# Performance work log

Measured on AMD Instinct MI355X. Metric: run time of the kernel, lower is better.

## Reference

```python
import jax, jax.numpy as jnp
import numpy as np

B, N, M, D = 1, 16384, 16384, 3
CHUNK = 2048          # x tile size for the online-min KNN pass
NN_WEIGHT = 1.0       # self.nn_weight
# both_ways=False, free_weight=0, ch_normals_K=0 -> only cham_x branch is active


def setup_inputs() -> dict:
    key = jax.random.key(0)
    k1, k2, k3 = jax.random.split(key, 3)
    # LiDAR-like point clouds, scaled to a ~20 m scene extent
    pc1 = jax.random.normal(k1, (B, N, D), dtype=jnp.float32) * 10.0
    est_flow = jax.random.normal(k2, (B, N, D), dtype=jnp.float32) * 0.1
    pc2 = jax.random.normal(k3, (B, M, D), dtype=jnp.float32) * 10.0
    return {"pc1": pc1, "est_flow": est_flow, "pc2": pc2}


def _knn1_l1_dists(x, y):
    """Per-point min L1 distance from x [N,3] to y [M,3], tiled over x.

    Equivalent to knn_points(x, y, K=1, norm=1).dists[..., 0] without
    materializing the full [N, M] distance matrix.
    """
    n = x.shape[0]
    x_tiles = x.reshape(n // CHUNK, CHUNK, D)

    def tile_min(xc):  # xc: [CHUNK, 3]
        d = jnp.sum(jnp.abs(xc[:, None, :] - y[None, :, :]), axis=-1)  # [CHUNK, M]
        return jnp.min(d, axis=-1)                                     # [CHUNK]

    return jax.lax.map(tile_min, x_tiles).reshape(n)


def reference(pc1, est_flow, pc2):
    x = pc1 + est_flow                                   # deformed cloud [B,N,3]
    cham_x = jax.vmap(_knn1_l1_dists)(x, pc2)            # [B, N]
    cham_y = jnp.float32(0.0)                            # both_ways=False
    freespace_loss = jnp.zeros_like(cham_x)              # free_weight == 0 branch
    chamf_loss = NN_WEIGHT * (cham_x.mean() + cham_y)    # free_weight * 0 omitted
    return (chamf_loss, freespace_loss)
```

## Files before the change

### kernel.cpp

```cpp
#include <hip/hip_runtime.h>


#define TPB 256
#define RB 8
#define PTS_PER_BLOCK (TPB * RB)
#define MSEG 128

__global__ __launch_bounds__(TPB) void chamfer_kernel(
    const float* __restrict__ pc1, const float* __restrict__ flow,
    const float* __restrict__ pc2, unsigned* __restrict__ minbits,
    int N, int M) {
    __shared__ float ysx[MSEG], ysy[MSEG], ysz[MSEG];

    const int t  = threadIdx.x;
    const int y0 = blockIdx.y * MSEG;
    const int len = (M - y0 < MSEG) ? (M - y0) : MSEG;

    for (int j = t; j < len; j += TPB) {
        const int g = y0 + j;
        ysx[j] = pc2[3 * g];
        ysy[j] = pc2[3 * g + 1];
        ysz[j] = pc2[3 * g + 2];
    }

    const int ibase = blockIdx.x * PTS_PER_BLOCK + t;
    float ax[RB], ay[RB], az[RB];
#pragma unroll
    for (int r = 0; r < RB; ++r) {
        const int i = ibase + r * TPB;
        const int ic = (i < N) ? i : (N - 1);
        ax[r] = pc1[3 * ic]     + flow[3 * ic];
        ay[r] = pc1[3 * ic + 1] + flow[3 * ic + 1];
        az[r] = pc1[3 * ic + 2] + flow[3 * ic + 2];
    }
    __syncthreads();

    float m[RB];
#pragma unroll
    for (int r = 0; r < RB; ++r) m[r] = 3.0e38f;

    if ((len & 3) == 0) {
        const float4* __restrict__ X4 = (const float4*)ysx;
        const float4* __restrict__ Y4 = (const float4*)ysy;
        const float4* __restrict__ Z4 = (const float4*)ysz;
#pragma unroll 2
        for (int q = 0; q < len / 4; ++q) {
            const float4 YX = X4[q];
            const float4 YY = Y4[q];
            const float4 YZ = Z4[q];
#pragma unroll
            for (int r = 0; r < RB; ++r) {
                const float d0 = fabsf(ax[r] - YX.x) + fabsf(ay[r] - YY.x) + fabsf(az[r] - YZ.x);
                const float d1 = fabsf(ax[r] - YX.y) + fabsf(ay[r] - YY.y) + fabsf(az[r] - YZ.y);
                const float d2 = fabsf(ax[r] - YX.z) + fabsf(ay[r] - YY.z) + fabsf(az[r] - YZ.z);
                const float d3 = fabsf(ax[r] - YX.w) + fabsf(ay[r] - YY.w) + fabsf(az[r] - YZ.w);
                m[r] = fminf(fminf(m[r], d0), d1);
                m[r] = fminf(fminf(m[r], d2), d3);
            }
        }
    } else {
        for (int j = 0; j < len; ++j) {
            const float yx = ysx[j], yy = ysy[j], yz = ysz[j];
#pragma unroll
            for (int r = 0; r < RB; ++r)
                m[r] = fminf(m[r], fabsf(ax[r] - yx) + fabsf(ay[r] - yy) + fabsf(az[r] - yz));
        }
    }

#pragma unroll
    for (int r = 0; r < RB; ++r) {
        const int i = ibase + r * TPB;
        if (i < N) atomicMin(&minbits[i], __float_as_uint(m[r]));
    }
}

__global__ __launch_bounds__(1024) void reduce_kernel(
    const unsigned* __restrict__ minbits, float* __restrict__ out, int N) {
    float s = 0.0f;
    const uint4* p = (const uint4*)minbits;
    for (int k = threadIdx.x; k < N / 4; k += 1024) {
        uint4 v = p[k];
        s += __uint_as_float(v.x) + __uint_as_float(v.y) +
             __uint_as_float(v.z) + __uint_as_float(v.w);
    }
    for (int k = (N / 4) * 4 + threadIdx.x; k < N; k += 1024)
        s += __uint_as_float(minbits[k]);
#pragma unroll
    for (int off = 32; off > 0; off >>= 1) s += __shfl_down(s, off, 64);
    __shared__ float ls[16];
    const int wid = threadIdx.x >> 6, lane = threadIdx.x & 63;
    if (lane == 0) ls[wid] = s;
    __syncthreads();
    if (threadIdx.x == 0) {
        float tot = 0.0f;
        for (int w = 0; w < 16; ++w) tot += ls[w];
        out[0] = tot / (float)N;
    }
}

extern "C" void kernel_launch(void* const* d_in, const int* in_sizes, int n_in,
                              void* d_out, int out_size, void* d_ws, size_t ws_size,
                              hipStream_t stream) {
    const float* pc1  = (const float*)d_in[0];
    const float* flow = (const float*)d_in[1];
    const float* pc2  = (const float*)d_in[2];
    float* out = (float*)d_out;

    const int N = in_sizes[0] / 3;
    const int M = in_sizes[2] / 3;

    unsigned* minbits = (unsigned*)d_ws;

    hipMemsetAsync(d_out, 0, (size_t)out_size * sizeof(float), stream);
    hipMemsetAsync(minbits, 0x7F, (size_t)N * sizeof(unsigned), stream);

    const int nbN    = (N + PTS_PER_BLOCK - 1) / PTS_PER_BLOCK;
    const int msplit = (M + MSEG - 1) / MSEG;

    chamfer_kernel<<<dim3(nbN, msplit), TPB, 0, stream>>>(pc1, flow, pc2, minbits, N, M);
    reduce_kernel<<<1, 1024, 0, stream>>>(minbits, out, N);
}
```

Before: 49.97 us.

## Use inline-asm abs-add/min3 distance kernel with software-pipelined LDS loads and RB=4

Replaces the compiler-generated L1 distance loop with inline GCN assembly that folds the abs into v_add operands and combines two distances per v_min3. The loop now loads the next float4 group from LDS while the current one is computed. Per-thread rows drop from 8 to 4 and launch bounds request 8 blocks per CU, trading register reuse of the y tile for higher occupancy. The shared arrays are padded so the prefetch one group past the end stays in bounds.

```diff
diff --git a/kernel.cpp b/kernel.cpp
--- a/kernel.cpp
+++ b/kernel.cpp
@@ -2,15 +2,45 @@
 
 
 #define TPB 256
-#define RB 8
+#define RB 4
 #define PTS_PER_BLOCK (TPB * RB)
 #define MSEG 128
 
-__global__ __launch_bounds__(TPB) void chamfer_kernel(
+#define DIST2(MR, AXv, AYv, AZv, Y0X, Y0Y, Y0Z, Y1X, Y1Y, Y1Z)            \
+  {                                                                        \
+    float t0, t1, t2, t3, t4;                                              \
+    asm("v_sub_f32 %1, %6, %9\n\t"                                         \
+        "v_sub_f32 %2, %7, %10\n\t"                                        \
+        "v_sub_f32 %3, %8, %11\n\t"                                        \
+        "v_sub_f32 %4, %6, %12\n\t"                                        \
+        "v_sub_f32 %5, %7, %13\n\t"                                        \
+        "v_add_f32 %1, |%1|, |%2|\n\t"                                     \
+        "v_sub_f32 %2, %8, %14\n\t"                                        \
+        "v_add_f32 %4, |%4|, |%5|\n\t"                                     \
+        "v_add_f32 %1, %1, |%3|\n\t"                                       \
+        "v_add_f32 %4, %4, |%2|\n\t"                                       \
+        "v_min3_f32 %0, %0, %1, %4"                                        \
+        : "+v"(MR), "=&v"(t0), "=&v"(t1), "=&v"(t2), "=&v"(t3), "=&v"(t4)  \
+        : "v"(AXv), "v"(AYv), "v"(AZv),                                    \
+          "v"(Y0X), "v"(Y0Y), "v"(Y0Z), "v"(Y1X), "v"(Y1Y), "v"(Y1Z));    \
+  }
+
+#define DIST8(Q4X, Q4Y, Q4Z)                                               \
+  {                                                                        \
+    _Pragma("unroll")                                                      \
+    for (int r = 0; r < RB; ++r) {                                         \
+      DIST2(m[r], ax[r], ay[r], az[r],                                     \
+            Q4X.x, Q4Y.x, Q4Z.x, Q4X.y, Q4Y.y, Q4Z.y);                     \
+      DIST2(m[r], ax[r], ay[r], az[r],                                     \
+            Q4X.z, Q4Y.z, Q4Z.z, Q4X.w, Q4Y.w, Q4Z.w);                     \
+    }                                                                      \
+  }
+
+__global__ __launch_bounds__(TPB, 8) void chamfer_kernel(
     const float* __restrict__ pc1, const float* __restrict__ flow,
     const float* __restrict__ pc2, unsigned* __restrict__ minbits,
     int N, int M) {
-    __shared__ float ysx[MSEG], ysy[MSEG], ysz[MSEG];
+    __shared__ float ysx[MSEG + 4], ysy[MSEG + 4], ysz[MSEG + 4];
 
     const int t  = threadIdx.x;
     const int y0 = blockIdx.y * MSEG;
@@ -39,24 +69,17 @@
 #pragma unroll
     for (int r = 0; r < RB; ++r) m[r] = 3.0e38f;
 
-    if ((len & 3) == 0) {
+    if ((len & 7) == 0) {
         const float4* __restrict__ X4 = (const float4*)ysx;
         const float4* __restrict__ Y4 = (const float4*)ysy;
         const float4* __restrict__ Z4 = (const float4*)ysz;
-#pragma unroll 2
-        for (int q = 0; q < len / 4; ++q) {
-            const float4 YX = X4[q];
-            const float4 YY = Y4[q];
-            const float4 YZ = Z4[q];
-#pragma unroll
-            for (int r = 0; r < RB; ++r) {
-                const float d0 = fabsf(ax[r] - YX.x) + fabsf(ay[r] - YY.x) + fabsf(az[r] - YZ.x);
-                const float d1 = fabsf(ax[r] - YX.y) + fabsf(ay[r] - YY.y) + fabsf(az[r] - YZ.y);
-                const float d2 = fabsf(ax[r] - YX.z) + fabsf(ay[r] - YY.z) + fabsf(az[r] - YZ.z);
-                const float d3 = fabsf(ax[r] - YX.w) + fabsf(ay[r] - YY.w) + fabsf(az[r] - YZ.w);
-                m[r] = fminf(fminf(m[r], d0), d1);
-                m[r] = fminf(fminf(m[r], d2), d3);
-            }
+        const int nq = len >> 2;
+        float4 aX = X4[0], aY = Y4[0], aZ = Z4[0];
+        for (int q = 0; q < nq; q += 2) {
+            float4 bX = X4[q + 1], bY = Y4[q + 1], bZ = Z4[q + 1];
+            DIST8(aX, aY, aZ);
+            aX = X4[q + 2]; aY = Y4[q + 2]; aZ = Z4[q + 2];
+            DIST8(bX, bY, bZ);
         }
     } else {
         for (int j = 0; j < len; ++j) {
```

Result: faster. 42.12 us (-15.7%).
